# Optimization experiments

Hardware: AMD Instinct MI355X
Metric: run time of the kernel (lower is better)

The kernel has to match this reference:

```python
import jax, jax.numpy as jnp
import numpy as np

# static video/block geometry (matches grid_sizes = [12, 30, 50], block_layout = (3, 5, 10))
F_, H_, W_ = 12, 30, 50
FB, HB, WB = 3, 5, 10
P1, P2, P3 = F_ // FB, H_ // HB, W_ // WB      # (4, 6, 5) -> 120 tokens per block
NB = FB * HB * WB                               # 150 blocks
B = 1
N = F_ * H_ * W_                                # 18000 tokens
DIM, NH = 1536, 12
HD = DIM // NH                                  # 128
CC = HD // 2                                    # 64 rotary pairs
SPLITS = (CC - 2 * (CC // 3), CC // 3, CC // 3) # (22, 21, 21) per torch split
EPS = 1e-6
MAXP = max(F_, H_, W_)


def _block_weight():
    # BlockDistanceConv3D with transform='linear': 1 - d/dmax, column-normalized (sum over dim=0)
    f, i, j = np.meshgrid(np.arange(FB), np.arange(HB), np.arange(WB), indexing='ij')
    centers = np.stack([f.ravel() + 0.5, i.ravel() + 0.5, j.ravel() + 0.5], 1).astype(np.float64)
    d = np.linalg.norm(centers[:, None] - centers[None, :], axis=-1)
    mat = 1.0 - d / d.max()
    mat = mat / mat.sum(axis=0, keepdims=True)
    return jnp.asarray(mat, jnp.float32)        # [NB, NB]

W_BLK = _block_weight()


def setup_inputs():
    key = jax.random.key(0)
    ks = jax.random.split(key, 10)
    x = jax.random.normal(ks[0], (B, N, DIM), jnp.float32)
    seq_lens = jnp.full((B,), N, jnp.int32)
    grid_sizes = jnp.tile(jnp.array([[F_, H_, W_]], jnp.int32), (B, 1))
    # rope freqs table [MAXP, CC]: per-axis sub-tables of widths SPLITS, base 1e4
    cols = []
    for sz in SPLITS:
        inv = 1.0 / (10000.0 ** (np.arange(sz, dtype=np.float64) / sz))
        cols.append(np.arange(MAXP)[:, None] * inv[None, :])
    ang = np.concatenate(cols, axis=1)
    freqs_cos = jnp.asarray(np.cos(ang), jnp.float32)
    freqs_sin = jnp.asarray(np.sin(ang), jnp.float32)
    s = 0.02
    wq = jax.random.normal(ks[1], (DIM, DIM), jnp.float32) * s
    wk = jax.random.normal(ks[2], (DIM, DIM), jnp.float32) * s
    wv = jax.random.normal(ks[3], (DIM, DIM), jnp.float32) * s
    wo = jax.random.normal(ks[4], (DIM, DIM), jnp.float32) * s
    bq = jax.random.normal(ks[5], (DIM,), jnp.float32) * 0.01
    bk = jax.random.normal(ks[6], (DIM,), jnp.float32) * 0.01
    bv = jax.random.normal(ks[7], (DIM,), jnp.float32) * 0.01
    bo = jnp.zeros((DIM,), jnp.float32)
    nq_w = 1.0 + 0.1 * jax.random.normal(ks[8], (DIM,), jnp.float32)
    nk_w = 1.0 + 0.1 * jax.random.normal(ks[9], (DIM,), jnp.float32)
    return dict(x=x, seq_lens=seq_lens, grid_sizes=grid_sizes,
                freqs_cos=freqs_cos, freqs_sin=freqs_sin,
                wq=wq, bq=bq, wk=wk, bk=bk, wv=wv, bv=bv, wo=wo, bo=bo,
                nq_w=nq_w, nk_w=nk_w)


def _rmsnorm(t, w):
    return t * jax.lax.rsqrt(jnp.mean(t * t, -1, keepdims=True) + EPS) * w


def _pos_tab(tab):
    # expand per-axis freq table into per-token table [N, CC] (f-major, then h, then w)
    c0, c1 = SPLITS[0], SPLITS[0] + SPLITS[1]
    f = jnp.broadcast_to(tab[:F_, :c0][:, None, None, :], (F_, H_, W_, SPLITS[0]))
    h = jnp.broadcast_to(tab[:H_, c0:c1][None, :, None, :], (F_, H_, W_, SPLITS[1]))
    w = jnp.broadcast_to(tab[:W_, c1:][None, None, :, :], (F_, H_, W_, SPLITS[2]))
    return jnp.concatenate([f, h, w], -1).reshape(N, CC)


def _rope(t, cos, sin):
    # complex multiply on interleaved pairs, real arithmetic: (x0+ix1)*(c+is)
    tr = t.reshape(B, N, NH, CC, 2)
    x0, x1 = tr[..., 0], tr[..., 1]
    c = cos[None, :, None, :]
    s = sin[None, :, None, :]
    return jnp.stack([x0 * c - x1 * s, x0 * s + x1 * c], -1).reshape(B, N, NH, HD)


def _to_blocks(t):
    # 'b (fb p1 hb p2 wb p3) h d -> (b h) (fb hb wb) (p1 p2 p3) d'
    t = t.reshape(B, FB, P1, HB, P2, WB, P3, NH, HD)
    t = t.transpose(0, 7, 1, 3, 5, 2, 4, 6, 8)
    return t.reshape(B * NH, NB, P1 * P2 * P3, HD)


def reference(x, seq_lens, grid_sizes, freqs_cos, freqs_sin,
              wq, bq, wk, bk, wv, bv, wo, bo, nq_w, nk_w):
    # qkv projections (float32 throughout, as torch upcasts q/k/v to float)
    q = x @ wq.T + bq
    k = x @ wk.T + bk
    v = x @ wv.T + bv
    # RMSNorm over full dim, then relu + eps (linear-attention positivity)
    q = jax.nn.relu(_rmsnorm(q, nq_w)) + EPS
    k = jax.nn.relu(_rmsnorm(k, nk_w)) + EPS
    q = q.reshape(B, N, NH, HD)
    k = k.reshape(B, N, NH, HD)
    v = v.reshape(B, N, NH, HD)
    pc, ps = _pos_tab(freqs_cos), _pos_tab(freqs_sin)
    q_rope = _rope(q, pc, ps)
    k_rope = _rope(k, pc, ps)
    qb, kb, vb, qrb, krb = map(_to_blocks, (q, k, v, q_rope, k_rope))
    # per-block linear attention state: kv[b,n] = k_rope^T @ v
    kv = jnp.einsum('bnpd,bnpe->bnde', krb, vb)           # [B*NH, NB, HD, HD]
    kv = jnp.einsum('oi,bide->bode', W_BLK, kv)            # block-distance mixing (1x1 conv)
    # normalizer: block_mix(q @ sum_p k)
    ksum = kb.sum(axis=2)                                  # [B*NH, NB, HD]
    qk = jnp.einsum('bnpd,bnd->bnp', qb, ksum)             # [B*NH, NB, P]
    norm = jnp.einsum('oi,bip->bop', W_BLK, qk)[..., None] + EPS
    out = jnp.einsum('bnpd,bnde->bnpe', qrb, kv) / norm    # [B*NH, NB, P, HD]
    # '(b h) n p d -> b (fb p1 hb p2 wb p3) (h d)'
    out = out.reshape(B, NH, FB, HB, WB, P1, P2, P3, HD)
    out = out.transpose(0, 2, 5, 3, 6, 4, 7, 1, 8).reshape(B, N, DIM)
    return out @ wo.T + bo
```

## Files before the change

### kernel.cpp

```cpp
#include <hip/hip_runtime.h>
#include <stdint.h>


typedef unsigned short u16;
typedef unsigned int   u32;

typedef _Float16 f16x8 __attribute__((ext_vector_type(8)));
typedef float    f32x4 __attribute__((ext_vector_type(4)));

#define N_TOK 18000
#define MPAD  18176
#define DIMD  1536
#define NHH   12
#define HD    128
#define CCH   64
#define QKVN  4608
#define NBLK  150
#define PBLK  120
#define EPSF  1e-6f

#define DEVFN static __device__ __forceinline__
#define AS1 __attribute__((address_space(1)))
#define AS3 __attribute__((address_space(3)))

DEVFN u16 f2h(float f){ _Float16 h = (_Float16)f; return __builtin_bit_cast(u16, h); }
DEVFN float h2f(u16 u){ _Float16 h = __builtin_bit_cast(_Float16, u); return (float)h; }
DEVFN int2 pack4h(float a,float b,float c,float d){
  int2 r;
  r.x = (int)((u32)f2h(a) | ((u32)f2h(b)<<16));
  r.y = (int)((u32)f2h(c) | ((u32)f2h(d)<<16));
  return r;
}
DEVFN int4 packi4(float4 lo4, float4 hi4){
  int2 lo = pack4h(lo4.x, lo4.y, lo4.z, lo4.w);
  int2 hi = pack4h(hi4.x, hi4.y, hi4.z, hi4.w);
  int4 r; r.x=lo.x; r.y=lo.y; r.z=hi.x; r.w=hi.y;
  return r;
}

DEVFN void gl_lds16(const u16* g, u16* l){
  __builtin_amdgcn_global_load_lds((const AS1 void*)g, (AS3 void*)l, 16, 0, 0);
}

DEVFN f32x4 mf(f16x8 a, f16x8 b, f32x4 c){
  return __builtin_amdgcn_mfma_f32_16x16x32_f16(a, b, c, 0, 0, 0);
}

DEVFN int tok_of(int b, int p){
  int fb = b/50, hb = (b/10)%5, wb = b%10;
  int p1 = p/30; int pr = p - p1*30; int p2 = pr/5, p3 = pr - p2*5;
  return (fb*4 + p1)*1500 + (hb*6 + p2)*50 + (wb*5 + p3);
}
DEVFN void tok_pos(int b, int p, int& tok, int& f, int& h2, int& w2){
  int fb = b/50, hb = (b/10)%5, wb = b%10;
  int p1 = p/30; int pr = p - p1*30; int p2 = pr/5, p3 = pr - p2*5;
  f = fb*4 + p1; h2 = hb*6 + p2; w2 = wb*5 + p3;
  tok = (f*30 + h2)*50 + w2;
}


__global__ void conv_x_k(const float* __restrict__ x, u16* __restrict__ xh){
  const long i = ((long)blockIdx.x*256 + threadIdx.x)*8;
  if (i >= (long)MPAD*DIMD) return;
  if (i < (long)N_TOK*DIMD){
    const float4 a = *(const float4*)(x + i);
    const float4 b = *(const float4*)(x + i + 4);
    *(int4*)(xh + i) = packi4(a, b);
  } else {
    *(int4*)(xh + i) = make_int4(0,0,0,0);
  }
}

__global__ void conv_w_k(const float* __restrict__ wq, const float* __restrict__ wk,
                         const float* __restrict__ wv, const float* __restrict__ wo,
                         const float* __restrict__ bq, const float* __restrict__ bk,
                         const float* __restrict__ bv,
                         u16* __restrict__ wqkvb, u16* __restrict__ wob, float* __restrict__ bqkv){
  const long i = (long)blockIdx.x*256 + threadIdx.x;
  const long idx = i*4;
  const long SQ = (long)DIMD*DIMD;
  const long WQKV = 3*SQ;
  if (idx < WQKV){
    const float* src = (idx < SQ) ? (wq + idx) : (idx < 2*SQ ? wk + (idx - SQ) : wv + (idx - 2*SQ));
    const float4 v = *(const float4*)src;
    *(int2*)(wqkvb + idx) = pack4h(v.x, v.y, v.z, v.w);
  } else if (idx < WQKV + SQ){
    const long j = idx - WQKV;
    const float4 v = *(const float4*)(wo + j);
    *(int2*)(wob + j) = pack4h(v.x, v.y, v.z, v.w);
  }
  if (i < 3*DIMD) bqkv[i] = (i < DIMD) ? bq[i] : (i < 2*DIMD ? bk[i - DIMD] : bv[i - 2*DIMD]);
}

__global__ void wblk_k(float* __restrict__ wblk, u16* __restrict__ wh){
  __shared__ double cs[NBLK];
  const int t = threadIdx.x;
  const double dmax = sqrt(101.0);
  if (t < NBLK){
    const int fi = t/50, hi = (t/10)%5, wi = t%10;
    double s = 0.0;
    for (int o = 0; o < NBLK; o++){
      const int fo = o/50, ho = (o/10)%5, wo = o%10;
      const int df = fo-fi, dh = ho-hi, dw = wo-wi;
      s += 1.0 - sqrt((double)(df*df + dh*dh + dw*dw))/dmax;
    }
    cs[t] = s;
  }
  __syncthreads();
  for (int idx = t; idx < NBLK*NBLK; idx += 256){
    const int o = idx/NBLK, i = idx%NBLK;
    const int fo = o/50, ho = (o/10)%5, wo = o%10;
    const int fi = i/50, hi = (i/10)%5, wi = i%10;
    const int df = fo-fi, dh = ho-hi, dw = wo-wi;
    const double v = 1.0 - sqrt((double)(df*df + dh*dh + dw*dw))/dmax;
    wblk[idx] = (float)(v / cs[i]);
  }
  for (int idx = t; idx < 160*160; idx += 256){
    const int o = idx/160, i = idx%160;
    u16 hv = 0;
    if (o < NBLK && i < NBLK){
      const int fo = o/50, ho = (o/10)%5, wo = o%10;
      const int fi = i/50, hi = (i/10)%5, wi = i%10;
      const int df = fo-fi, dh = ho-hi, dw = wo-wi;
      const double v = 1.0 - sqrt((double)(df*df + dh*dh + dw*dw))/dmax;
      hv = f2h((float)(v / cs[i]));
    }
    wh[idx] = hv;
  }
}


#define STG_A(bB, kt, h) { const int ko_ = (kt)*64 + (h)*32; \
  gl_lds16(Aat + offA0 + ko_, lds + (bB)*32768 + (h)*8192 + t*8); \
  gl_lds16(Aat + offA1 + ko_, lds + (bB)*32768 + (h)*8192 + t*8 + 4096); }
#define STG_B(bB, kt, h) { const int ko_ = (kt)*64 + (h)*32; \
  gl_lds16(Bat + offB0 + ko_, lds + (bB)*32768 + 16384 + (h)*8192 + t*8); \
  gl_lds16(Bat + offB1 + ko_, lds + (bB)*32768 + 16384 + (h)*8192 + t*8 + 4096); }
#define VMC(n) asm volatile("s_waitcnt vmcnt(" #n ")" ::: "memory")
#define BARR() __builtin_amdgcn_s_barrier()
#define LGK0() asm volatile("s_waitcnt lgkmcnt(0)" ::: "memory")

#define PH_ODD(bB, kk, STG) { \
  const u16* ab_ = lds + (bB)*32768 + (kk)*8192 + arow; \
  const u16* bb_ = lds + (bB)*32768 + 16384 + (kk)*8192 + brow; \
  _Pragma("unroll") for (int mt_=0; mt_<8; mt_++) aF[mt_] = *(const f16x8*)(ab_ + mt_*512); \
  bF[0] = *(const f16x8*)(bb_); bF[1] = *(const f16x8*)(bb_ + 512); \
  STG; BARR(); LGK0(); \
  __builtin_amdgcn_s_setprio(1); \
  _Pragma("unroll") for (int mt_=0; mt_<8; mt_++){ \
    acc[mt_][0] = mf(aF[mt_], bF[0], acc[mt_][0]); \
    acc[mt_][1] = mf(aF[mt_], bF[1], acc[mt_][1]); } \
  __builtin_amdgcn_s_setprio(0); BARR(); }

#define PH_EVEN(bB, kk, STG) { \
  const u16* bb_ = lds + (bB)*32768 + 16384 + (kk)*8192 + brow; \
  bF[2] = *(const f16x8*)(bb_ + 1024); bF[3] = *(const f16x8*)(bb_ + 1536); \
  STG; BARR(); LGK0(); \
  __builtin_amdgcn_s_setprio(1); \
  _Pragma("unroll") for (int mt_=0; mt_<8; mt_++){ \
    acc[mt_][2] = mf(aF[mt_], bF[2], acc[mt_][2]); \
    acc[mt_][3] = mf(aF[mt_], bF[3], acc[mt_][3]); } \
  __builtin_amdgcn_s_setprio(0); BARR(); }

DEVFN void gemm256_core(const u16* __restrict__ Aat, const u16* __restrict__ Bat,
                        u16* lds, long row0, long col0, int K, f32x4 (&acc)[8][4]){
  const int t = threadIdx.x;
  const int lane = t&63, lr = lane&15, q = lane>>4;
  const int w = t>>6, wr = w>>2, wc = w&3;
  const int slot8 = (q ^ ((lr>>1)&3))*8;
  const int arow = (wr*128 + lr)*32 + slot8;
  const int brow = (wc*64 + lr)*32 + slot8;
  const int s1 = t + 512;
  const int r0 = t>>2, r1 = s1>>2;
  const int g0 = ((t&3)  ^ ((r0>>1)&3))*8;
  const int g1 = ((s1&3) ^ ((r1>>1)&3))*8;
  const long offA0 = (row0 + r0)*(long)K + g0, offA1 = (row0 + r1)*(long)K + g1;
  const long offB0 = (col0 + r0)*(long)K + g0, offB1 = (col0 + r1)*(long)K + g1;

  f16x8 aF[8], bF[4];
  STG_A(0,0,0); STG_B(0,0,0); STG_A(0,0,1); STG_B(0,0,1);
  STG_A(1,1,0); STG_B(1,1,0); STG_A(1,1,1);
  VMC(6); BARR();

  const int NIT = K/128;
#pragma unroll 1
  for (int j = 0; j < NIT-1; ++j){
    const int c1 = 2*j+1, p0 = 2*j+2, p1 = 2*j+3;
    PH_ODD (0,0, STG_B(1,c1,1));
    PH_EVEN(0,0, STG_A(0,p0,0));
    PH_ODD (0,1, STG_B(0,p0,0));
    PH_EVEN(0,1, { STG_A(0,p0,1); VMC(6); });
    PH_ODD (1,0, STG_B(0,p0,1));
    PH_EVEN(1,0, STG_A(1,p1,0));
    PH_ODD (1,1, STG_B(1,p1,0));
    PH_EVEN(1,1, { STG_A(1,p1,1); VMC(6); });
  }
  { const int c1 = 2*(K/128)-1;
    PH_ODD (0,0, STG_B(1,c1,1));
    PH_EVEN(0,0, );
    PH_ODD (0,1, );
    PH_EVEN(0,1, VMC(0));
    PH_ODD (1,0, );
    PH_EVEN(1,0, );
    PH_ODD (1,1, );
    PH_EVEN(1,1, );
  }
}

__global__ __launch_bounds__(512, 2) void gemm_qkv256(const u16* __restrict__ A, const u16* __restrict__ B,
                                                      const float* __restrict__ bias,
                                                      u16* __restrict__ qb, u16* __restrict__ kb,
                                                      u16* __restrict__ vb){
  __shared__ u16 lds[65536];
  const int bn = blockIdx.x, bm = blockIdx.y;
  const long row0 = (long)bm*256, col0 = (long)bn*256;
  f32x4 acc[8][4] = {};
  gemm256_core(A, B, lds, row0, col0, DIMD, acc);

  const int t = threadIdx.x, lane = t&63, lr = lane&15, q = lane>>4;
  const int w = t>>6, wr = w>>2, wc = w&3;
  const int which = bn/6;
  u16* dst = (which == 0) ? qb : (which == 1 ? kb : vb);
  const int lcol0 = (bn - which*6)*256 + wc*64;
  const int gcol0 = bn*256 + wc*64;
#pragma unroll
  for (int nt = 0; nt < 4; nt++){
    const float bb = bias[gcol0 + nt*16 + lr];
    const int col = lcol0 + nt*16 + lr;
#pragma unroll
    for (int mt = 0; mt < 8; mt++)
#pragma unroll
      for (int r = 0; r < 4; r++){
        const long rr = row0 + wr*128 + mt*16 + q*4 + r;
        if (rr < N_TOK) dst[rr*DIMD + col] = f2h(acc[mt][nt][r] + bb);
      }
  }
}

__global__ __launch_bounds__(512, 2) void gemm_bt256(const u16* __restrict__ A, const u16* __restrict__ B,
                                                     const float* __restrict__ bias, float* __restrict__ C){
  __shared__ u16 lds[65536];
  const int bn = blockIdx.x, bm = blockIdx.y;
  const long row0 = (long)bm*256, col0 = (long)bn*256;
  f32x4 acc[8][4] = {};
  gemm256_core(A, B, lds, row0, col0, DIMD, acc);

  const int t = threadIdx.x, lane = t&63, lr = lane&15, q = lane>>4;
  const int w = t>>6, wr = w>>2, wc = w&3;
#pragma unroll
  for (int nt = 0; nt < 4; nt++){
    const int col = bn*256 + wc*64 + nt*16 + lr;
    const float bb = bias[col];
#pragma unroll
    for (int mt = 0; mt < 8; mt++)
#pragma unroll
      for (int r = 0; r < 4; r++){
        const long rr = row0 + wr*128 + mt*16 + q*4 + r;
        if (rr < N_TOK) C[rr*DIMD + col] = acc[mt][nt][r] + bb;
      }
  }
}

__global__ __launch_bounds__(256) void norm_k(u16* __restrict__ qb, u16* __restrict__ kb,
                                              const float* __restrict__ nqw, const float* __restrict__ nkw){
  __shared__ float red[4];
  __shared__ float s_scale;
  const int n = blockIdx.x, t = threadIdx.x, lane = t&63, wv = t>>6;
  u16* bufs[2]; bufs[0] = qb; bufs[1] = kb;
  const float* wgts[2]; wgts[0] = nqw; wgts[1] = nkw;
  for (int pass = 0; pass < 2; pass++){
    u16* row = bufs[pass] + (long)n*DIMD;
    const float* wgt = wgts[pass];
    float v[6];
    float ssq = 0.f;
#pragma unroll
    for (int i = 0; i < 6; i++){ v[i] = h2f(row[t + i*256]); ssq += v[i]*v[i]; }
#pragma unroll
    for (int o = 32; o > 0; o >>= 1) ssq += __shfl_down(ssq, o);
    if (lane == 0) red[wv] = ssq;
    __syncthreads();
    if (t == 0) s_scale = rsqrtf((red[0]+red[1]+red[2]+red[3])/(float)DIMD + EPSF);
    __syncthreads();
    const float sc = s_scale;
#pragma unroll
    for (int i = 0; i < 6; i++){
      float r = fmaxf(v[i]*sc*wgt[t + i*256], 0.f) + EPSF;
      row[t + i*256] = f2h(r);
    }
    __syncthreads();
  }
}

__global__ __launch_bounds__(128) void ksum_k(const u16* __restrict__ kb, float* __restrict__ ksum){
  const int hb = blockIdx.x; const int h = hb/NBLK, b = hb%NBLK; const int d = threadIdx.x;
  float s = 0.f;
  for (int p = 0; p < PBLK; p++)
    s += h2f(kb[(long)tok_of(b, p)*DIMD + h*HD + d]);
  ksum[(long)hb*HD + d] = s;
}

__global__ __launch_bounds__(128) void qk_k(const u16* __restrict__ qb, const float* __restrict__ ksum,
                                            float* __restrict__ qk){
  __shared__ float ks[HD];
  const int hb = blockIdx.x, h = hb/NBLK, b = hb%NBLK, t = threadIdx.x;
  ks[t] = ksum[(long)hb*HD + t];
  __syncthreads();
  if (t < PBLK){
    const u16* row = qb + (long)tok_of(b, t)*DIMD + h*HD;
    float s = 0.f;
#pragma unroll
    for (int d8 = 0; d8 < 16; d8++){
      int4 v4 = *(const int4*)(row + d8*8);
      const u16* pv = (const u16*)&v4;
#pragma unroll
      for (int j = 0; j < 8; j++) s += h2f(pv[j])*ks[d8*8 + j];
    }
    qk[(long)hb*PBLK + t] = s;
  }
}

__global__ __launch_bounds__(128) void mixqk_k(const float* __restrict__ qk, const float* __restrict__ wblk,
                                               float* __restrict__ nrm){
  const int ho = blockIdx.x, h = ho/NBLK, o = ho%NBLK, t = threadIdx.x;
  if (t >= PBLK) return;
  float s = 0.f;
  for (int i = 0; i < NBLK; i++) s += wblk[o*NBLK + i]*qk[((long)h*NBLK + i)*PBLK + t];
  nrm[(long)ho*PBLK + t] = s + EPSF;
}

__global__ __launch_bounds__(256) void kv_k(const u16* __restrict__ kb, const u16* __restrict__ vb,
                                            const float* __restrict__ fcos, const float* __restrict__ fsin,
                                            u16* __restrict__ kv1){
  __shared__ u16 Ap[4][128][32];
  __shared__ u16 Bp[4][128][32];
  const int hb = blockIdx.x, h = hb/NBLK, b = hb%NBLK, t = threadIdx.x;
  for (int idx = t; idx < 128*64; idx += 256){
    const int p = idx>>6, cc = idx&63;
    u16 v0=0, v1=0, r0=0, r1=0;
    if (p < PBLK){
      int tok, f, hh, ww; tok_pos(b, p, tok, f, hh, ww);
      const long tb = (long)tok*DIMD + h*HD + 2*cc;
      const u32 vv = *(const u32*)&vb[tb];
      const u32 kk = *(const u32*)&kb[tb];
      const int pos = (cc < 22) ? f : (cc < 43 ? hh : ww);
      const float cv = fcos[pos*CCH + cc], sv = fsin[pos*CCH + cc];
      const float x0 = h2f((u16)kk), x1 = h2f((u16)(kk>>16));
      v0 = (u16)vv; v1 = (u16)(vv>>16);
      r0 = f2h(x0*cv - x1*sv); r1 = f2h(x0*sv + x1*cv);
    }
    const int kp = p>>5, j = p&31;
    Ap[kp][2*cc][j] = v0; Ap[kp][2*cc+1][j] = v1;
    Bp[kp][2*cc][j] = r0; Bp[kp][2*cc+1][j] = r1;
  }
  __syncthreads();
  const int wave = t>>6, lane = t&63, lr = lane&15, quad = lane>>4;
  const int wm = (wave&1)*64, wn = (wave>>1)*64;
  f32x4 acc[4][4] = {};
#pragma unroll
  for (int kp = 0; kp < 4; kp++){
    f16x8 aF[4], bF[4];
#pragma unroll
    for (int mt = 0; mt < 4; mt++) aF[mt] = *(const f16x8*)&Ap[kp][wm + mt*16 + lr][quad*8];
#pragma unroll
    for (int nt = 0; nt < 4; nt++) bF[nt] = *(const f16x8*)&Bp[kp][wn + nt*16 + lr][quad*8];
#pragma unroll
    for (int mt = 0; mt < 4; mt++)
#pragma unroll
      for (int nt = 0; nt < 4; nt++)
        acc[mt][nt] = __builtin_amdgcn_mfma_f32_16x16x32_f16(aF[mt], bF[nt], acc[mt][nt], 0, 0, 0);
  }
  u16* outp = kv1 + (long)hb*HD*HD;
#pragma unroll
  for (int mt = 0; mt < 4; mt++)
#pragma unroll
    for (int nt = 0; nt < 4; nt++)
#pragma unroll
      for (int r = 0; r < 4; r++)
        outp[(wm + mt*16 + quad*4 + r)*HD + wn + nt*16 + lr] = f2h(acc[mt][nt][r]);
}

__global__ __launch_bounds__(256) void mix_gemm(const u16* __restrict__ kv1, const u16* __restrict__ wh,
                                                u16* __restrict__ kv2){
  __shared__ u16 Xs[5][128][32];
  const int h = blockIdx.y, jc = blockIdx.x, t = threadIdx.x;
  const long base = (long)h*NBLK*HD*HD + jc*128;
#pragma unroll
  for (int it = 0; it < 10; it++){
    const int idx = t + it*256;
    const int i = idx>>4, jg = idx&15;
    int4 v = make_int4(0,0,0,0);
    if (i < NBLK) v = *(const int4*)&kv1[base + (long)i*HD*HD + jg*8];
    const u16* pv = (const u16*)&v;
    const int kp = i>>5, il = i&31;
    const int ib = ((((il>>3) ^ jg) & 3)<<3) | (il&7);
#pragma unroll
    for (int e = 0; e < 8; e++) Xs[kp][jg*8 + e][ib] = pv[e];
  }
  __syncthreads();
  const int wave = t>>6, lane = t&63, lr = lane&15, quad = lane>>4;
  const int wm = (wave&1)*80, wn = (wave>>1)*64;
  f32x4 acc[5][4] = {};
#pragma unroll
  for (int kp = 0; kp < 5; kp++){
    f16x8 aF[5], bF[4];
#pragma unroll
    for (int mt = 0; mt < 5; mt++)
      aF[mt] = *(const f16x8*)&wh[(wm + mt*16 + lr)*160 + kp*32 + quad*8];
#pragma unroll
    for (int nt = 0; nt < 4; nt++){
      const int j = wn + nt*16 + lr;
      bF[nt] = *(const f16x8*)&Xs[kp][j][((quad ^ (j>>3)) & 3)<<3];
    }
#pragma unroll
    for (int mt = 0; mt < 5; mt++)
#pragma unroll
      for (int nt = 0; nt < 4; nt++)
        acc[mt][nt] = __builtin_amdgcn_mfma_f32_16x16x32_f16(aF[mt], bF[nt], acc[mt][nt], 0, 0, 0);
  }
#pragma unroll
  for (int mt = 0; mt < 5; mt++)
#pragma unroll
    for (int nt = 0; nt < 4; nt++)
#pragma unroll
      for (int r = 0; r < 4; r++){
        const int o = wm + mt*16 + quad*4 + r;
        if (o < NBLK)
          kv2[(long)(h*NBLK + o)*HD*HD + jc*128 + wn + nt*16 + lr] = f2h(acc[mt][nt][r]);
      }
}

__global__ __launch_bounds__(256) void attn_k(const u16* __restrict__ qb, const u16* __restrict__ kv2,
                                              const float* __restrict__ fcos, const float* __restrict__ fsin,
                                              const float* __restrict__ nrm, u16* __restrict__ aout){
  __shared__ u16 Ap[4][128][32];
  __shared__ u16 Bp[4][128][32];
  const int ho = blockIdx.x, h = ho/NBLK, o = ho%NBLK, t = threadIdx.x;
  for (int idx = t; idx < 128*64; idx += 256){
    const int p = idx>>6, cc = idx&63;
    u32 w = 0;
    if (p < PBLK){
      int tok, f, hh, ww; tok_pos(o, p, tok, f, hh, ww);
      const u32 qq = *(const u32*)&qb[(long)tok*DIMD + h*HD + 2*cc];
      const int pos = (cc < 22) ? f : (cc < 43 ? hh : ww);
      const float cv = fcos[pos*CCH + cc], sv = fsin[pos*CCH + cc];
      const float x0 = h2f((u16)qq), x1 = h2f((u16)(qq>>16));
      w = (u32)f2h(x0*cv - x1*sv) | ((u32)f2h(x0*sv + x1*cv) << 16);
    }
    *(u32*)&Ap[(2*cc)>>5][p][(2*cc)&31] = w;
  }
  const u16* kv2p = kv2 + (long)ho*HD*HD;
  for (int idx = t; idx < 128*16; idx += 256){
    const int e = idx>>4, d8 = (idx&15)*8;
    int4 vv = *(const int4*)&kv2p[e*HD + d8];
    *(int4*)&Bp[d8>>5][e][d8&31] = vv;
  }
  __syncthreads();
  const int wave = t>>6, lane = t&63, lr = lane&15, quad = lane>>4;
  const int wm = (wave&1)*64, wn = (wave>>1)*64;
  f32x4 acc[4][4] = {};
#pragma unroll
  for (int kp = 0; kp < 4; kp++){
    f16x8 aF[4], bF[4];
#pragma unroll
    for (int mt = 0; mt < 4; mt++) aF[mt] = *(const f16x8*)&Ap[kp][wm + mt*16 + lr][quad*8];
#pragma unroll
    for (int nt = 0; nt < 4; nt++) bF[nt] = *(const f16x8*)&Bp[kp][wn + nt*16 + lr][quad*8];
#pragma unroll
    for (int mt = 0; mt < 4; mt++)
#pragma unroll
      for (int nt = 0; nt < 4; nt++)
        acc[mt][nt] = __builtin_amdgcn_mfma_f32_16x16x32_f16(aF[mt], bF[nt], acc[mt][nt], 0, 0, 0);
  }
#pragma unroll
  for (int mt = 0; mt < 4; mt++)
#pragma unroll
    for (int r = 0; r < 4; r++){
      const int p = wm + mt*16 + quad*4 + r;
      if (p >= PBLK) continue;
      const float inv = 1.0f / nrm[(long)ho*PBLK + p];
      const long tb = (long)tok_of(o, p)*DIMD + h*HD;
#pragma unroll
      for (int nt = 0; nt < 4; nt++)
        aout[tb + wn + nt*16 + lr] = f2h(acc[mt][nt][r]*inv);
    }
}

extern "C" void kernel_launch(void* const* d_in, const int* in_sizes, int n_in,
                              void* d_out, int out_size, void* d_ws, size_t ws_size,
                              hipStream_t stream){
  const float* x    = (const float*)d_in[0];
  const float* fcos = (const float*)d_in[3];
  const float* fsin = (const float*)d_in[4];
  const float* wq   = (const float*)d_in[5];
  const float* bq   = (const float*)d_in[6];
  const float* wk   = (const float*)d_in[7];
  const float* bk   = (const float*)d_in[8];
  const float* wv   = (const float*)d_in[9];
  const float* bv   = (const float*)d_in[10];
  const float* wo   = (const float*)d_in[11];
  const float* bo   = (const float*)d_in[12];
  const float* nqw  = (const float*)d_in[13];
  const float* nkw  = (const float*)d_in[14];
  float* out = (float*)d_out;
  (void)in_sizes; (void)n_in; (void)out_size; (void)ws_size;

  char* ws = (char*)d_ws; size_t off = 0;
  auto alloc = [&](size_t b)->void*{ void* p = ws + off; off += (b + 255) & ~(size_t)255; return p; };
  const size_t SQ = (size_t)DIMD*DIMD;
  u16*   wqkvb = (u16*)  alloc(3*SQ*2);
  u16*   wob   = (u16*)  alloc(SQ*2);
  float* bqkv  = (float*)alloc((size_t)3*DIMD*4);
  float* wblk  = (float*)alloc((size_t)NBLK*NBLK*4);
  u16*   wh    = (u16*)  alloc((size_t)160*160*2);
  u16*   qb    = (u16*)  alloc((size_t)MPAD*DIMD*2);
  u16*   kb    = (u16*)  alloc((size_t)MPAD*DIMD*2);
  u16*   vb    = (u16*)  alloc((size_t)MPAD*DIMD*2);
  u16*   kv1   = (u16*)  alloc((size_t)NHH*NBLK*HD*HD*2);
  float* ksum  = (float*)alloc((size_t)NHH*NBLK*HD*4);
  float* qk    = (float*)alloc((size_t)NHH*NBLK*PBLK*4);
  float* nrm   = (float*)alloc((size_t)NHH*NBLK*PBLK*4);
  u16*   kv2   = kb;
  u16*   xh    = kv1;

  conv_w_k<<<9216, 256, 0, stream>>>(wq, wk, wv, wo, bq, bk, bv, wqkvb, wob, bqkv);
  wblk_k<<<1, 256, 0, stream>>>(wblk, wh);
  conv_x_k<<<(MPAD*DIMD/8 + 255)/256, 256, 0, stream>>>(x, xh);
  gemm_qkv256<<<dim3(QKVN/256, MPAD/256), 512, 0, stream>>>(xh, wqkvb, bqkv, qb, kb, vb);
  norm_k<<<N_TOK, 256, 0, stream>>>(qb, kb, nqw, nkw);
  ksum_k<<<NHH*NBLK, 128, 0, stream>>>(kb, ksum);
  qk_k<<<NHH*NBLK, 128, 0, stream>>>(qb, ksum, qk);
  mixqk_k<<<NHH*NBLK, 128, 0, stream>>>(qk, wblk, nrm);
  kv_k<<<NHH*NBLK, 256, 0, stream>>>(kb, vb, fcos, fsin, kv1);
  mix_gemm<<<dim3(HD*HD/128, NHH), 256, 0, stream>>>(kv1, wh, kv2);
  attn_k<<<NHH*NBLK, 256, 0, stream>>>(qb, kv2, fcos, fsin, nrm, qb);
  gemm_bt256<<<dim3(DIMD/256, MPAD/256), 512, 0, stream>>>(qb, wob, bo, out);
}
```

Measured before the change: 1.064 ms.

## Restructure GEMM main loop into 4-quadrant tiles with partial LDS waits

Reorganizes the 256x256 GEMM inner loop from 8 odd/even phases into TILE4 blocks. Each block reads A and B fragments in 4x4 quadrants into double register sets and uses graded lgkmcnt waits plus sched_barrier, so MFMAs can start before all LDS reads finish. The global-to-LDS staging order and vmcnt thresholds change to match. This raises register use (16 fragment vectors instead of 12) in exchange for better overlap of LDS reads with MFMA, and it carries some risk of wrong staging or wait counts.

```diff
diff --git a/kernel.cpp b/kernel.cpp
--- a/kernel.cpp
+++ b/kernel.cpp
@@ -138,34 +138,38 @@
   gl_lds16(Bat + offB1 + ko_, lds + (bB)*32768 + 16384 + (h)*8192 + t*8 + 4096); }
 #define VMC(n) asm volatile("s_waitcnt vmcnt(" #n ")" ::: "memory")
 #define BARR() __builtin_amdgcn_s_barrier()
-#define LGK0() asm volatile("s_waitcnt lgkmcnt(0)" ::: "memory")
-
-#define PH_ODD(bB, kk, STG) { \
-  const u16* ab_ = lds + (bB)*32768 + (kk)*8192 + arow; \
-  const u16* bb_ = lds + (bB)*32768 + 16384 + (kk)*8192 + brow; \
-  _Pragma("unroll") for (int mt_=0; mt_<8; mt_++) aF[mt_] = *(const f16x8*)(ab_ + mt_*512); \
-  bF[0] = *(const f16x8*)(bb_); bF[1] = *(const f16x8*)(bb_ + 512); \
-  STG; BARR(); LGK0(); \
+#define LGK(n) { asm volatile("s_waitcnt lgkmcnt(" #n ")" ::: "memory"); \
+                 __builtin_amdgcn_sched_barrier(0); }
+
+#define RD_A4(dst, bB, kk, mlo) { \
+  _Pragma("unroll") for (int i_=0;i_<4;i_++) \
+    dst[i_] = *(const f16x8*)(lds + (bB)*32768 + (kk)*8192 + arow + ((mlo)+i_)*512); }
+#define RD_B4(dst, bB, kk) { \
+  _Pragma("unroll") for (int i_=0;i_<4;i_++) \
+    dst[i_] = *(const f16x8*)(lds + (bB)*32768 + 16384 + (kk)*8192 + brow + i_*512); }
+#define MM4(mlo, aR, bR) { \
   __builtin_amdgcn_s_setprio(1); \
-  _Pragma("unroll") for (int mt_=0; mt_<8; mt_++){ \
-    acc[mt_][0] = mf(aF[mt_], bF[0], acc[mt_][0]); \
-    acc[mt_][1] = mf(aF[mt_], bF[1], acc[mt_][1]); } \
-  __builtin_amdgcn_s_setprio(0); BARR(); }
-
-#define PH_EVEN(bB, kk, STG) { \
-  const u16* bb_ = lds + (bB)*32768 + 16384 + (kk)*8192 + brow; \
-  bF[2] = *(const f16x8*)(bb_ + 1024); bF[3] = *(const f16x8*)(bb_ + 1536); \
-  STG; BARR(); LGK0(); \
-  __builtin_amdgcn_s_setprio(1); \
-  _Pragma("unroll") for (int mt_=0; mt_<8; mt_++){ \
-    acc[mt_][2] = mf(aF[mt_], bF[2], acc[mt_][2]); \
-    acc[mt_][3] = mf(aF[mt_], bF[3], acc[mt_][3]); } \
-  __builtin_amdgcn_s_setprio(0); BARR(); }
+  _Pragma("unroll") for (int i_=0;i_<4;i_++){ \
+    acc[(mlo)+i_][0] = mf(aR[i_], bR[0], acc[(mlo)+i_][0]); \
+    acc[(mlo)+i_][1] = mf(aR[i_], bR[1], acc[(mlo)+i_][1]); \
+    acc[(mlo)+i_][2] = mf(aR[i_], bR[2], acc[(mlo)+i_][2]); \
+    acc[(mlo)+i_][3] = mf(aR[i_], bR[3], acc[(mlo)+i_][3]); } \
+  __builtin_amdgcn_s_setprio(0); }
+
+#define TILE4(bB, S1, S2, S3, S4, VM) { \
+  RD_A4(aA, bB, 0, 0); RD_B4(bX, bB, 0); RD_A4(aB, bB, 0, 4); \
+  S1; LGK(4); MM4(0, aA, bX); BARR(); \
+  RD_A4(aA, bB, 1, 0); RD_B4(bY, bB, 1); \
+  S2; LGK(8); MM4(4, aB, bX); BARR(); \
+  RD_A4(aB, bB, 1, 4); \
+  S3; LGK(4); MM4(0, aA, bY); BARR(); \
+  S4; VM; LGK(0); MM4(4, aB, bY); BARR(); }
 
 DEVFN void gemm256_core(const u16* __restrict__ Aat, const u16* __restrict__ Bat,
                         u16* lds, long row0, long col0, int K, f32x4 (&acc)[8][4]){
   const int t = threadIdx.x;
-  const int lane = t&63, lr = lane&15, q = lane>>4;
+  const int lane = t&63, lr = lane&15;
+  const int q = lane>>4;
   const int w = t>>6, wr = w>>2, wc = w&3;
   const int slot8 = (q ^ ((lr>>1)&3))*8;
   const int arow = (wr*128 + lr)*32 + slot8;
@@ -177,33 +181,21 @@
   const long offA0 = (row0 + r0)*(long)K + g0, offA1 = (row0 + r1)*(long)K + g1;
   const long offB0 = (col0 + r0)*(long)K + g0, offB1 = (col0 + r1)*(long)K + g1;
 
-  f16x8 aF[8], bF[4];
+  f16x8 aA[4], aB[4], bX[4], bY[4];
   STG_A(0,0,0); STG_B(0,0,0); STG_A(0,0,1); STG_B(0,0,1);
-  STG_A(1,1,0); STG_B(1,1,0); STG_A(1,1,1);
-  VMC(6); BARR();
+  STG_A(1,1,0); STG_B(1,1,0);
+  VMC(4); BARR();
 
   const int NIT = K/128;
 #pragma unroll 1
   for (int j = 0; j < NIT-1; ++j){
     const int c1 = 2*j+1, p0 = 2*j+2, p1 = 2*j+3;
-    PH_ODD (0,0, STG_B(1,c1,1));
-    PH_EVEN(0,0, STG_A(0,p0,0));
-    PH_ODD (0,1, STG_B(0,p0,0));
-    PH_EVEN(0,1, { STG_A(0,p0,1); VMC(6); });
-    PH_ODD (1,0, STG_B(0,p0,1));
-    PH_EVEN(1,0, STG_A(1,p1,0));
-    PH_ODD (1,1, STG_B(1,p1,0));
-    PH_EVEN(1,1, { STG_A(1,p1,1); VMC(6); });
-  }
-  { const int c1 = 2*(K/128)-1;
-    PH_ODD (0,0, STG_B(1,c1,1));
-    PH_EVEN(0,0, );
-    PH_ODD (0,1, );
-    PH_EVEN(0,1, VMC(0));
-    PH_ODD (1,0, );
-    PH_EVEN(1,0, );
-    PH_ODD (1,1, );
-    PH_EVEN(1,1, );
+    TILE4(0, STG_A(1,c1,1), STG_B(1,c1,1), STG_A(0,p0,0), STG_B(0,p0,0), VMC(4));
+    TILE4(1, STG_A(0,p0,1), STG_B(0,p0,1), STG_A(1,p1,0), STG_B(1,p1,0), VMC(4));
+  }
+  { const int cL1 = 2*(K/128)-1;
+    TILE4(0, STG_A(1,cL1,1), STG_B(1,cL1,1), (void)0, (void)0, VMC(0));
+    TILE4(1, (void)0, (void)0, (void)0, (void)0, (void)0);
   }
 }
 
```

Result: no change. 1.048 ms (-1.5%).
